# Performance work log

Hardware: AMD Instinct MI355X
Metric: run time of the kernel (lower is better)

The kernel has to match this reference:

```python
import jax, jax.numpy as jnp
import numpy as np

X_DIM = 1024
HEADS = 16
EPS = 1e-5  # torch LayerNorm default


def setup_inputs() -> dict:
    key = jax.random.key(0)
    ks = jax.random.split(key, 4)
    B, N = 4, 1024
    x = jax.random.normal(ks[0], (B, N, X_DIM), jnp.float32)
    # torch nn.Linear weights are [out_features, in_features]; y = x @ W.T
    Wq = jax.random.normal(ks[1], (X_DIM, X_DIM), jnp.float32) * 0.02
    Wkv = jax.random.normal(ks[2], (2 * X_DIM, X_DIM), jnp.float32) * 0.02  # k_dim = x_dim + v_dim
    Wt = jax.random.normal(ks[3], (HEADS, HEADS), jnp.float32) * 0.25  # talk_h head-mixing
    ln_g = jnp.ones((HEADS,), jnp.float32)
    ln_b = jnp.zeros((HEADS,), jnp.float32)
    return {"x": x, "Wq": Wq, "Wkv": Wkv, "Wt": Wt, "ln_g": ln_g, "ln_b": ln_b}


def reference(x, Wq, Wkv, Wt, ln_g, ln_b):
    B, N, D = x.shape
    H = HEADS
    dh = D // H  # v head dim (= x head dim here since v_dim == x_dim)
    # projections
    q = (x @ Wq.T).reshape(B, N, H, dh).transpose(0, 2, 1, 3)  # b h i d
    kv = x @ Wkv.T  # [B, N, 2D]
    k = kv[..., :D].reshape(B, N, H, dh).transpose(0, 2, 1, 3)  # b h j d
    v = kv[..., D:].reshape(B, N, H, dh).transpose(0, 2, 1, 3)  # b h j d
    # scaled dot-product scores (scale uses x_dim, not head dim — faithful to source)
    dots = jnp.einsum('bhid,bhjd->bhij', q, k) * (D ** -0.5)
    w = jax.nn.softmax(dots, axis=-1)  # [B, H, N, N]
    # talk_h: ChSwap (transpose dims 1 and -1) -> Linear(heads) -> LayerNorm(heads) -> ChSwap
    wt = w.transpose(0, 3, 2, 1)  # b j i h
    wt = wt @ Wt.T
    mu = wt.mean(-1, keepdims=True)
    var = wt.var(-1, keepdims=True)
    wt = (wt - mu) / jnp.sqrt(var + EPS) * ln_g + ln_b
    w = wt.transpose(0, 3, 2, 1)  # back to b h i j
    # soft attention output
    attn = jnp.einsum('bhij,bhjd->bhid', w, v)
    # hard selection: argmax over keys, gather value rows
    idx = jnp.argmax(w, axis=-1)  # [B, H, N]
    hard = jnp.take_along_axis(v, jnp.broadcast_to(idx[..., None], idx.shape + (dh,)), axis=2)
    # straight-through: forward = hard, gradient flows through attn
    rtn = attn - jax.lax.stop_gradient(attn - hard)
    return rtn.transpose(0, 2, 1, 3).reshape(B, N, H * dh)
```

## Files before the change

### kernel.cpp

```cpp
#include <hip/hip_runtime.h>


#define FMA4(cc, av, bv) \
  cc.x = fmaf(av, bv.x, cc.x); cc.y = fmaf(av, bv.y, cc.y); \
  cc.z = fmaf(av, bv.z, cc.z); cc.w = fmaf(av, bv.w, cc.w);

__global__ __launch_bounds__(256) void qkv_gemm(
    const float* __restrict__ X, const float* __restrict__ Wq,
    const float* __restrict__ Wkv, float* __restrict__ qT,
    float* __restrict__ kT, float* __restrict__ V)
{
  __shared__ __align__(16) float As[16 * 132];
  __shared__ __align__(16) float Bs[16 * 132];
  __shared__ __align__(16) float tb[128 * 32];

  const int t  = threadIdx.x;
  const int bn = blockIdx.x;
  const int bm = blockIdx.y;
  const int m0 = bm * 128, n0 = bn * 128;
  const int ty = t >> 4, tx = t & 15;

  const float* Wbase = (n0 < 1024) ? Wq : Wkv;
  const int nw0 = (n0 < 1024) ? n0 : (n0 - 1024);

  float4 c2[8][2];
#pragma unroll
  for (int a = 0; a < 8; a++) {
    c2[a][0] = make_float4(0.f, 0.f, 0.f, 0.f);
    c2[a][1] = make_float4(0.f, 0.f, 0.f, 0.f);
  }

  const int lr = t >> 1;
  const int lh = t & 1;

  const float4* As4 = (const float4*)As;
  const float4* Bs4 = (const float4*)Bs;

  for (int kb = 0; kb < 64; kb++) {
    const int k0 = kb * 16;
    __syncthreads();
#pragma unroll
    for (int s = 0; s < 2; s++) {
      const int kk = lh * 8 + s * 4;
      float4 av = *(const float4*)&X[(size_t)(m0 + lr) * 1024 + k0 + kk];
      float4 bv = *(const float4*)&Wbase[(size_t)(nw0 + lr) * 1024 + k0 + kk];
      As[(kk + 0) * 132 + lr] = av.x;
      As[(kk + 1) * 132 + lr] = av.y;
      As[(kk + 2) * 132 + lr] = av.z;
      As[(kk + 3) * 132 + lr] = av.w;
      Bs[(kk + 0) * 132 + lr] = bv.x;
      Bs[(kk + 1) * 132 + lr] = bv.y;
      Bs[(kk + 2) * 132 + lr] = bv.z;
      Bs[(kk + 3) * 132 + lr] = bv.w;
    }
    __syncthreads();
#pragma unroll
    for (int kk = 0; kk < 16; kk++) {
      float4 a0 = As4[kk * 33 + ty * 2];
      float4 a1 = As4[kk * 33 + ty * 2 + 1];
      float4 b0 = Bs4[kk * 33 + tx];
      float4 b1 = Bs4[kk * 33 + 16 + tx];
      FMA4(c2[0][0], a0.x, b0); FMA4(c2[0][1], a0.x, b1);
      FMA4(c2[1][0], a0.y, b0); FMA4(c2[1][1], a0.y, b1);
      FMA4(c2[2][0], a0.z, b0); FMA4(c2[2][1], a0.z, b1);
      FMA4(c2[3][0], a0.w, b0); FMA4(c2[3][1], a0.w, b1);
      FMA4(c2[4][0], a1.x, b0); FMA4(c2[4][1], a1.x, b1);
      FMA4(c2[5][0], a1.y, b0); FMA4(c2[5][1], a1.y, b1);
      FMA4(c2[6][0], a1.z, b0); FMA4(c2[6][1], a1.z, b1);
      FMA4(c2[7][0], a1.w, b0); FMA4(c2[7][1], a1.w, b1);
    }
  }

  if (n0 >= 2048) {
    const int nv0 = n0 - 2048;
#pragma unroll
    for (int a = 0; a < 8; a++) {
      *(float4*)&V[(size_t)(m0 + ty * 8 + a) * 1024 + nv0 + tx * 4]      = c2[a][0];
      *(float4*)&V[(size_t)(m0 + ty * 8 + a) * 1024 + nv0 + 64 + tx * 4] = c2[a][1];
    }
    return;
  }

  float* T = (n0 < 1024) ? qT : kT;
  const int nt0 = (n0 < 1024) ? n0 : (n0 - 1024);
  const int bB = m0 >> 10;
  const int i0 = m0 & 1023;
#pragma unroll
  for (int r = 0; r < 4; r++) {
    __syncthreads();
    if ((tx >> 3) == (r & 1)) {
      const int c0 = (tx & 7) * 4;
#pragma unroll
      for (int a = 0; a < 8; a++) {
        const int m = ty * 8 + a;
        float4 val = c2[a][r >> 1];
        tb[m * 32 + ((c0 + 0 + m) & 31)] = val.x;
        tb[m * 32 + ((c0 + 1 + m) & 31)] = val.y;
        tb[m * 32 + ((c0 + 2 + m) & 31)] = val.z;
        tb[m * 32 + ((c0 + 3 + m) & 31)] = val.w;
      }
    }
    __syncthreads();
    const int nl = t >> 3, mq = t & 7;
    float* Trow = T + (size_t)(bB * 1024 + nt0 + (r >> 1) * 64 + (r & 1) * 32 + nl) * 1024 + i0;
#pragma unroll
    for (int l = 0; l < 4; l++) {
      const int mb = (l * 8 + mq) * 4;
      float4 o;
      o.x = tb[(mb + 0) * 32 + ((nl + mb + 0) & 31)];
      o.y = tb[(mb + 1) * 32 + ((nl + mb + 1) & 31)];
      o.z = tb[(mb + 2) * 32 + ((nl + mb + 2) & 31)];
      o.w = tb[(mb + 3) * 32 + ((nl + mb + 3) & 31)];
      *(float4*)(Trow + mb) = o;
    }
  }
}

__global__ __launch_bounds__(256) void attn_stats_v5(
    const float* __restrict__ qT, const float* __restrict__ kT,
    float* __restrict__ Mm, float* __restrict__ Ml)
{
  const int t  = threadIdx.x;
  const int bx = blockIdx.x;
  const int b  = bx >> 8;
  const int it = (bx >> 3) & 31;
  const int js = bx & 7;
  const int wv = t >> 6;
  const int l  = t & 63;
  const int ih = l >> 5;
  const int jg = l & 31;
  const int i0w = __builtin_amdgcn_readfirstlane(it * 32 + wv * 8);
  const int iq = i0w + ih * 4;
  const int jq = js * 128 + jg * 4;

  const float scale = 0.03125f;

  for (int h = 0; h < 16; h++) {
    const size_t base = (size_t)(b * 1024 + h * 64) * 1024;
    float4 acc[4];
#pragma unroll
    for (int ii = 0; ii < 4; ii++) acc[ii] = make_float4(0.f, 0.f, 0.f, 0.f);

#pragma unroll 4
    for (int d = 0; d < 64; d++) {
      const float4 qv = *(const float4*)(qT + base + (size_t)d * 1024 + iq);
      const float4 kv = *(const float4*)(kT + base + (size_t)d * 1024 + jq);
      FMA4(acc[0], qv.x, kv);
      FMA4(acc[1], qv.y, kv);
      FMA4(acc[2], qv.z, kv);
      FMA4(acc[3], qv.w, kv);
    }

#pragma unroll
    for (int ii = 0; ii < 4; ii++) {
      const float s0 = acc[ii].x * scale;
      const float s1 = acc[ii].y * scale;
      const float s2 = acc[ii].z * scale;
      const float s3 = acc[ii].w * scale;
      float mx = fmaxf(fmaxf(s0, s1), fmaxf(s2, s3));
      mx = fmaxf(mx, __shfl_xor(mx, 1));
      mx = fmaxf(mx, __shfl_xor(mx, 2));
      mx = fmaxf(mx, __shfl_xor(mx, 4));
      mx = fmaxf(mx, __shfl_xor(mx, 8));
      mx = fmaxf(mx, __shfl_xor(mx, 16));
      float ss = __expf(s0 - mx) + __expf(s1 - mx) +
                 __expf(s2 - mx) + __expf(s3 - mx);
      ss += __shfl_xor(ss, 1);
      ss += __shfl_xor(ss, 2);
      ss += __shfl_xor(ss, 4);
      ss += __shfl_xor(ss, 8);
      ss += __shfl_xor(ss, 16);
      if (jg == ii) {
        const int idx = (((b * 16 + h) * 1024 + iq + ii) << 3) + js;
        Mm[idx] = mx;
        Ml[idx] = ss;
      }
    }
  }
}

__device__ inline unsigned long long mkkey(float v, int j) {
  unsigned u = __float_as_uint(v);
  u = (u & 0x80000000u) ? ~u : (u | 0x80000000u);
  return ((unsigned long long)u << 32) | (unsigned)(1023 - j);
}

__global__ __launch_bounds__(256) void attn_select_v5(
    const float* __restrict__ qT, const float* __restrict__ kT,
    const float* __restrict__ Mm, const float* __restrict__ Ml,
    const float* __restrict__ Wt, const float* __restrict__ ln_g,
    const float* __restrict__ ln_b, unsigned long long* __restrict__ HiKey)
{
  __shared__ __align__(16) float smem[64 * 271 + 512];
  float* ptile = smem;
  float* mred  = smem + 64 * 271;
  float* rred  = mred + 256;

  const int t  = threadIdx.x;
  const int bx = blockIdx.x;
  const int b  = bx >> 10;
  const int it = (bx >> 4) & 63;
  const int js = bx & 15;
  const int i0 = it << 4;
  const int j0 = js << 6;

  const float scale = 0.03125f;

  {
    const int base = (((b * 16 + (t >> 4)) * 1024 + i0 + (t & 15)) << 3);
    const float4 ma = *(const float4*)&Mm[base];
    const float4 mb = *(const float4*)&Mm[base + 4];
    const float4 la = *(const float4*)&Ml[base];
    const float4 lb = *(const float4*)&Ml[base + 4];
    float M = fmaxf(fmaxf(fmaxf(ma.x, ma.y), fmaxf(ma.z, ma.w)),
                    fmaxf(fmaxf(mb.x, mb.y), fmaxf(mb.z, mb.w)));
    float L = la.x * __expf(ma.x - M) + la.y * __expf(ma.y - M) +
              la.z * __expf(ma.z - M) + la.w * __expf(ma.w - M) +
              lb.x * __expf(mb.x - M) + lb.y * __expf(mb.y - M) +
              lb.z * __expf(mb.z - M) + lb.w * __expf(mb.w - M);
    mred[t] = M;
    rred[t] = 1.0f / L;
  }
  __syncthreads();

  const int wv = t >> 6;
  const int l  = t & 63;
  const int jq = l & 15;
  const int ig = l >> 4;
  const int iq = i0 + ig * 4;
  const int jcol = j0 + jq * 4;

#pragma unroll
  for (int hl = 0; hl < 4; hl++) {
    const int h = wv * 4 + hl;
    const size_t base = (size_t)(b * 1024 + h * 64) * 1024;
    float4 acc[4];
#pragma unroll
    for (int ii = 0; ii < 4; ii++) acc[ii] = make_float4(0.f, 0.f, 0.f, 0.f);

#pragma unroll 4
    for (int d = 0; d < 64; d++) {
      const float4 qv = *(const float4*)(qT + base + (size_t)d * 1024 + iq);
      const float4 kv = *(const float4*)(kT + base + (size_t)d * 1024 + jcol);
      FMA4(acc[0], qv.x, kv);
      FMA4(acc[1], qv.y, kv);
      FMA4(acc[2], qv.z, kv);
      FMA4(acc[3], qv.w, kv);
    }

    const int hrot = (h + jq) & 15;
#pragma unroll
    for (int ii = 0; ii < 4; ii++) {
      const int iL = ig * 4 + ii;
      const float m = mred[h * 16 + iL];
      const float r = rred[h * 16 + iL];
      const float a4[4] = {acc[ii].x, acc[ii].y, acc[ii].z, acc[ii].w};
#pragma unroll
      for (int jj = 0; jj < 4; jj++) {
        const int j = jq * 4 + jj;
        const float p = __expf(a4[jj] * scale - m) * r;
        ptile[j * 271 + iL * 17 + hrot] = p;
      }
    }
  }
  __syncthreads();

  const int i2 = t >> 4;
  const int g  = (t >> 2) & 3;
  const int hq = t & 3;

  float wtr[4][16], gr[4], br[4];
#pragma unroll
  for (int a = 0; a < 4; a++) {
#pragma unroll
    for (int h2 = 0; h2 < 16; h2++) wtr[a][h2] = Wt[(hq * 4 + a) * 16 + h2];
    gr[a] = ln_g[hq * 4 + a];
    br[a] = ln_b[hq * 4 + a];
  }
  float bv[4]; int bix[4];
#pragma unroll
  for (int a = 0; a < 4; a++) { bv[a] = -1e30f; bix[a] = 0; }

#pragma unroll
  for (int jj = 0; jj < 16; jj++) {
    const int j = g * 16 + jj;
    const int jr = j >> 2;
    float pv[16];
#pragma unroll
    for (int h2 = 0; h2 < 16; h2++)
      pv[h2] = ptile[j * 271 + i2 * 17 + ((h2 + jr) & 15)];
    float mix[4];
#pragma unroll
    for (int a = 0; a < 4; a++) {
      float s0 = 0.f;
#pragma unroll
      for (int h2 = 0; h2 < 16; h2++) s0 = fmaf(pv[h2], wtr[a][h2], s0);
      mix[a] = s0;
    }
    float s1 = mix[0] + mix[1] + mix[2] + mix[3];
    s1 += __shfl_xor(s1, 1);
    s1 += __shfl_xor(s1, 2);
    const float mu = s1 * 0.0625f;
    float s2 = 0.f;
#pragma unroll
    for (int a = 0; a < 4; a++) { const float dd = mix[a] - mu; s2 = fmaf(dd, dd, s2); }
    s2 += __shfl_xor(s2, 1);
    s2 += __shfl_xor(s2, 2);
    const float rstd = rsqrtf(s2 * 0.0625f + 1e-5f);
    const int jg2 = j0 + j;
#pragma unroll
    for (int a = 0; a < 4; a++) {
      const float nv = (mix[a] - mu) * rstd * gr[a] + br[a];
      if (nv > bv[a]) { bv[a] = nv; bix[a] = jg2; }
    }
  }

#pragma unroll
  for (int a = 0; a < 4; a++) {
    float v = bv[a]; int ix = bix[a];
    {
      const float ov = __shfl_xor(v, 4);
      const int oi = __shfl_xor(ix, 4);
      if (ov > v || (ov == v && oi < ix)) { v = ov; ix = oi; }
    }
    {
      const float ov = __shfl_xor(v, 8);
      const int oi = __shfl_xor(ix, 8);
      if (ov > v || (ov == v && oi < ix)) { v = ov; ix = oi; }
    }
    bv[a] = v; bix[a] = ix;
  }

  if (g == 0) {
#pragma unroll
    for (int a = 0; a < 4; a++) {
      const int cell = (b * 16 + hq * 4 + a) * 1024 + i0 + i2;
      atomicMax(&HiKey[cell], mkkey(bv[a], bix[a]));
    }
  }
}

__global__ __launch_bounds__(256) void gather_v4(
    const unsigned long long* __restrict__ HiKey, const float* __restrict__ V,
    float* __restrict__ out)
{
  const int t  = threadIdx.x;
  const int bx = blockIdx.x;
  const int b  = bx >> 6;
  const int it = bx & 63;
  const int i2 = t >> 4;
  const int h  = t & 15;

  const unsigned long long key = HiKey[(b * 16 + h) * 1024 + it * 16 + i2];
  const int j = 1023 - (int)(unsigned)(key & 0xFFFFFFFFull);

  const float* vs = V + (size_t)(b * 1024 + j) * 1024 + h * 64;
  float* dst = out + (size_t)(b * 1024 + it * 16 + i2) * 1024 + h * 64;
#pragma unroll
  for (int w = 0; w < 16; w++)
    *(float4*)(dst + w * 4) = *(const float4*)(vs + w * 4);
}

extern "C" void kernel_launch(void* const* d_in, const int* in_sizes, int n_in,
                              void* d_out, int out_size, void* d_ws, size_t ws_size,
                              hipStream_t stream) {
  const float* x   = (const float*)d_in[0];
  const float* Wq  = (const float*)d_in[1];
  const float* Wkv = (const float*)d_in[2];
  const float* Wt  = (const float*)d_in[3];
  const float* lng = (const float*)d_in[4];
  const float* lnb = (const float*)d_in[5];
  float* out = (float*)d_out;
  float* ws  = (float*)d_ws;
  float* qT = ws;
  float* kT = ws + (size_t)4 * 1024 * 1024;
  float* V  = ws + (size_t)8 * 1024 * 1024;
  float* Mm = ws + (size_t)12 * 1024 * 1024;
  float* Ml = Mm + 524288;
  unsigned long long* HiKey =
      (unsigned long long*)(ws + (size_t)13 * 1024 * 1024);

  hipLaunchKernelGGL(qkv_gemm, dim3(24, 32), dim3(256), 0, stream,
                     x, Wq, Wkv, qT, kT, V);
  hipMemsetAsync(HiKey, 0, (size_t)65536 * 8, stream);
  hipLaunchKernelGGL(attn_stats_v5, dim3(1024), dim3(256), 0, stream,
                     qT, kT, Mm, Ml);
  hipLaunchKernelGGL(attn_select_v5, dim3(4096), dim3(256), 0, stream,
                     qT, kT, Mm, Ml, Wt, lng, lnb, HiKey);
  hipLaunchKernelGGL(gather_v4, dim3(256), dim3(256), 0, stream,
                     HiKey, V, out);
}
```

Before: 955.9 us.

## Materialize exp scores in stats pass and reuse them in select pass

The stats kernel now writes the exponentiated, max-shifted scores to a large workspace buffer (B*H*N*N floats). The select kernel reads these instead of recomputing the QK^T dot products, and rescales them by per-split softmax correction factors before the head-mixing, LayerNorm and argmax step. This removes the second QK^T computation but adds 256MB of global writes plus reads, so the kernel becomes memory-bound. It is used only when the workspace is large enough; otherwise the old path runs.

```diff
diff --git a/kernel.cpp b/kernel.cpp
--- a/kernel.cpp
+++ b/kernel.cpp
@@ -179,6 +179,74 @@
   }
 }
 
+__global__ __launch_bounds__(256) void attn_stats_v6(
+    const float* __restrict__ qT, const float* __restrict__ kT,
+    float* __restrict__ Mm, float* __restrict__ Ml, float* __restrict__ Sp)
+{
+  const int t  = threadIdx.x;
+  const int bx = blockIdx.x;
+  const int b  = bx >> 8;
+  const int it = (bx >> 3) & 31;
+  const int js = bx & 7;
+  const int wv = t >> 6;
+  const int l  = t & 63;
+  const int ih = l >> 5;
+  const int jg = l & 31;
+  const int i0w = __builtin_amdgcn_readfirstlane(it * 32 + wv * 8);
+  const int iq = i0w + ih * 4;
+  const int jq = js * 128 + jg * 4;
+
+  const float scale = 0.03125f;
+
+  for (int h = 0; h < 16; h++) {
+    const size_t base = (size_t)(b * 1024 + h * 64) * 1024;
+    float4 acc[4];
+#pragma unroll
+    for (int ii = 0; ii < 4; ii++) acc[ii] = make_float4(0.f, 0.f, 0.f, 0.f);
+
+#pragma unroll 4
+    for (int d = 0; d < 64; d++) {
+      const float4 qv = *(const float4*)(qT + base + (size_t)d * 1024 + iq);
+      const float4 kv = *(const float4*)(kT + base + (size_t)d * 1024 + jq);
+      FMA4(acc[0], qv.x, kv);
+      FMA4(acc[1], qv.y, kv);
+      FMA4(acc[2], qv.z, kv);
+      FMA4(acc[3], qv.w, kv);
+    }
+
+#pragma unroll
+    for (int ii = 0; ii < 4; ii++) {
+      const float s0 = acc[ii].x * scale;
+      const float s1 = acc[ii].y * scale;
+      const float s2 = acc[ii].z * scale;
+      const float s3 = acc[ii].w * scale;
+      float mx = fmaxf(fmaxf(s0, s1), fmaxf(s2, s3));
+      mx = fmaxf(mx, __shfl_xor(mx, 1));
+      mx = fmaxf(mx, __shfl_xor(mx, 2));
+      mx = fmaxf(mx, __shfl_xor(mx, 4));
+      mx = fmaxf(mx, __shfl_xor(mx, 8));
+      mx = fmaxf(mx, __shfl_xor(mx, 16));
+      const float e0 = __expf(s0 - mx);
+      const float e1 = __expf(s1 - mx);
+      const float e2 = __expf(s2 - mx);
+      const float e3 = __expf(s3 - mx);
+      *(float4*)&Sp[((size_t)((b * 16 + h) * 1024) + iq + ii) * 1024 + jq] =
+          make_float4(e0, e1, e2, e3);
+      float ss = e0 + e1 + e2 + e3;
+      ss += __shfl_xor(ss, 1);
+      ss += __shfl_xor(ss, 2);
+      ss += __shfl_xor(ss, 4);
+      ss += __shfl_xor(ss, 8);
+      ss += __shfl_xor(ss, 16);
+      if (jg == ii) {
+        const int idx = (((b * 16 + h) * 1024 + iq + ii) << 3) + js;
+        Mm[idx] = mx;
+        Ml[idx] = ss;
+      }
+    }
+  }
+}
+
 __device__ inline unsigned long long mkkey(float v, int j) {
   unsigned u = __float_as_uint(v);
   u = (u & 0x80000000u) ? ~u : (u | 0x80000000u);
@@ -261,6 +329,141 @@
         const float p = __expf(a4[jj] * scale - m) * r;
         ptile[j * 271 + iL * 17 + hrot] = p;
       }
+    }
+  }
+  __syncthreads();
+
+  const int i2 = t >> 4;
+  const int g  = (t >> 2) & 3;
+  const int hq = t & 3;
+
+  float wtr[4][16], gr[4], br[4];
+#pragma unroll
+  for (int a = 0; a < 4; a++) {
+#pragma unroll
+    for (int h2 = 0; h2 < 16; h2++) wtr[a][h2] = Wt[(hq * 4 + a) * 16 + h2];
+    gr[a] = ln_g[hq * 4 + a];
+    br[a] = ln_b[hq * 4 + a];
+  }
+  float bv[4]; int bix[4];
+#pragma unroll
+  for (int a = 0; a < 4; a++) { bv[a] = -1e30f; bix[a] = 0; }
+
+#pragma unroll
+  for (int jj = 0; jj < 16; jj++) {
+    const int j = g * 16 + jj;
+    const int jr = j >> 2;
+    float pv[16];
+#pragma unroll
+    for (int h2 = 0; h2 < 16; h2++)
+      pv[h2] = ptile[j * 271 + i2 * 17 + ((h2 + jr) & 15)];
+    float mix[4];
+#pragma unroll
+    for (int a = 0; a < 4; a++) {
+      float s0 = 0.f;
+#pragma unroll
+      for (int h2 = 0; h2 < 16; h2++) s0 = fmaf(pv[h2], wtr[a][h2], s0);
+      mix[a] = s0;
+    }
+    float s1 = mix[0] + mix[1] + mix[2] + mix[3];
+    s1 += __shfl_xor(s1, 1);
+    s1 += __shfl_xor(s1, 2);
+    const float mu = s1 * 0.0625f;
+    float s2 = 0.f;
+#pragma unroll
+    for (int a = 0; a < 4; a++) { const float dd = mix[a] - mu; s2 = fmaf(dd, dd, s2); }
+    s2 += __shfl_xor(s2, 1);
+    s2 += __shfl_xor(s2, 2);
+    const float rstd = rsqrtf(s2 * 0.0625f + 1e-5f);
+    const int jg2 = j0 + j;
+#pragma unroll
+    for (int a = 0; a < 4; a++) {
+      const float nv = (mix[a] - mu) * rstd * gr[a] + br[a];
+      if (nv > bv[a]) { bv[a] = nv; bix[a] = jg2; }
+    }
+  }
+
+#pragma unroll
+  for (int a = 0; a < 4; a++) {
+    float v = bv[a]; int ix = bix[a];
+    {
+      const float ov = __shfl_xor(v, 4);
+      const int oi = __shfl_xor(ix, 4);
+      if (ov > v || (ov == v && oi < ix)) { v = ov; ix = oi; }
+    }
+    {
+      const float ov = __shfl_xor(v, 8);
+      const int oi = __shfl_xor(ix, 8);
+      if (ov > v || (ov == v && oi < ix)) { v = ov; ix = oi; }
+    }
+    bv[a] = v; bix[a] = ix;
+  }
+
+  if (g == 0) {
+#pragma unroll
+    for (int a = 0; a < 4; a++) {
+      const int cell = (b * 16 + hq * 4 + a) * 1024 + i0 + i2;
+      atomicMax(&HiKey[cell], mkkey(bv[a], bix[a]));
+    }
+  }
+}
+
+__global__ __launch_bounds__(256) void attn_select_v11(
+    const float* __restrict__ Sp,
+    const float* __restrict__ Mm, const float* __restrict__ Ml,
+    const float* __restrict__ Wt, const float* __restrict__ ln_g,
+    const float* __restrict__ ln_b, unsigned long long* __restrict__ HiKey)
+{
+  __shared__ __align__(16) float smem[64 * 271 + 256];
+  float* ptile = smem;
+  float* fred  = smem + 64 * 271;
+
+  const int t  = threadIdx.x;
+  const int bx = blockIdx.x;
+  const int b  = bx >> 10;
+  const int it = (bx >> 4) & 63;
+  const int js = bx & 15;
+  const int i0 = it << 4;
+  const int j0 = js << 6;
+
+  {
+    const int base = (((b * 16 + (t >> 4)) * 1024 + i0 + (t & 15)) << 3);
+    const float4 ma = *(const float4*)&Mm[base];
+    const float4 mb = *(const float4*)&Mm[base + 4];
+    const float4 la = *(const float4*)&Ml[base];
+    const float4 lb = *(const float4*)&Ml[base + 4];
+    float M = fmaxf(fmaxf(fmaxf(ma.x, ma.y), fmaxf(ma.z, ma.w)),
+                    fmaxf(fmaxf(mb.x, mb.y), fmaxf(mb.z, mb.w)));
+    float L = la.x * __expf(ma.x - M) + la.y * __expf(ma.y - M) +
+              la.z * __expf(ma.z - M) + la.w * __expf(ma.w - M) +
+              lb.x * __expf(mb.x - M) + lb.y * __expf(mb.y - M) +
+              lb.z * __expf(mb.z - M) + lb.w * __expf(mb.w - M);
+    const int si = js >> 1;
+    const float4 mv = (si & 4) ? mb : ma;
+    const int s2 = si & 3;
+    const float msl = (s2 == 0) ? mv.x : (s2 == 1) ? mv.y
+                    : (s2 == 2) ? mv.z : mv.w;
+    fred[t] = __expf(msl - M) / L;
+  }
+  __syncthreads();
+
+#pragma unroll
+  for (int rr = 0; rr < 8; rr++) {
+    const int rowid = rr * 32 + (t >> 3);
+    const int h  = rowid >> 4;
+    const int iL = rowid & 15;
+    const int jseg = (t & 7) * 8;
+    const float f = fred[rowid];
+    const float* src = Sp + ((size_t)(b * 16 + h) * 1024 + i0 + iL) * 1024
+                          + j0 + jseg;
+    const float4 e0 = *(const float4*)src;
+    const float4 e1 = *(const float4*)(src + 4);
+    const float pv8[8] = {e0.x * f, e0.y * f, e0.z * f, e0.w * f,
+                          e1.x * f, e1.y * f, e1.z * f, e1.w * f};
+#pragma unroll
+    for (int k = 0; k < 8; k++) {
+      const int j = jseg + k;
+      ptile[j * 271 + iL * 17 + ((h + (j >> 2)) & 15)] = pv8[k];
     }
   }
   __syncthreads();
@@ -379,14 +582,25 @@
   float* Ml = Mm + 524288;
   unsigned long long* HiKey =
       (unsigned long long*)(ws + (size_t)13 * 1024 * 1024);
+  float* Sp = ws + (size_t)14 * 1024 * 1024;
+
+  const size_t NEED = (size_t)78 * 1024 * 1024 * 4;
+  const bool big_ws = (ws_size >= NEED);
 
   hipLaunchKernelGGL(qkv_gemm, dim3(24, 32), dim3(256), 0, stream,
                      x, Wq, Wkv, qT, kT, V);
   hipMemsetAsync(HiKey, 0, (size_t)65536 * 8, stream);
-  hipLaunchKernelGGL(attn_stats_v5, dim3(1024), dim3(256), 0, stream,
-                     qT, kT, Mm, Ml);
-  hipLaunchKernelGGL(attn_select_v5, dim3(4096), dim3(256), 0, stream,
-                     qT, kT, Mm, Ml, Wt, lng, lnb, HiKey);
+  if (big_ws) {
+    hipLaunchKernelGGL(attn_stats_v6, dim3(1024), dim3(256), 0, stream,
+                       qT, kT, Mm, Ml, Sp);
+    hipLaunchKernelGGL(attn_select_v11, dim3(4096), dim3(256), 0, stream,
+                       Sp, Mm, Ml, Wt, lng, lnb, HiKey);
+  } else {
+    hipLaunchKernelGGL(attn_stats_v5, dim3(1024), dim3(256), 0, stream,
+                       qT, kT, Mm, Ml);
+    hipLaunchKernelGGL(attn_select_v5, dim3(4096), dim3(256), 0, stream,
+                       qT, kT, Mm, Ml, Wt, lng, lnb, HiKey);
+  }
   hipLaunchKernelGGL(gather_v4, dim3(256), dim3(256), 0, stream,
                      HiKey, V, out);
 }
```

New measurement: 978.9 us. 2.4% more time.
